# Kernel optimization log

Hardware: AMD Instinct MI355X
Metric: run time of the kernel (lower is better)

The kernel has to match this reference:

```python
import jax, jax.numpy as jnp
import numpy as np

EPS = 1e-4

def setup_inputs() -> dict:
    key = jax.random.key(0)
    k1, k2, k3 = jax.random.split(key, 3)
    batch, keysize, dict_size, categories = 4096, 512, 16384, 100
    x = jax.random.normal(k1, (batch, keysize), dtype=jnp.float32)
    keys = jax.random.normal(k2, (dict_size, keysize), dtype=jnp.float32) * 0.1  # TruncatedNormal(0, 0.1) approx
    values = jax.random.uniform(k3, (dict_size, categories), dtype=jnp.float32)
    return {"x": x, "keys": keys, "values": values}


def reference(x, keys, values):
    # sq_distance(keys, x): (dict_size, batch)
    kk = jnp.sum(keys * keys, axis=1)[:, None]          # (D, 1)
    xx = jnp.sum(x * x, axis=1)[None, :]                # (1, B)
    d = kk - 2.0 * jnp.matmul(keys, x.T) + xx           # (D, B)
    kern = 1.0 / (d + EPS)                              # reciprocal kernel
    # transpose -> (B, D), matmul values (D, C) -> (B, C)
    return jnp.matmul(kern.T, values)
```

## Files before the change

kernel.cpp:

```cpp
#include <hip/hip_runtime.h>
#include <hip/hip_bf16.h>
#include <hip/hip_fp8.h>
#include <cstdint>


#define BSZ   4096
#define DSZ   16384
#define KSZ   512
#define CC    100
#define CP    128
#define EPSV  1e-4f

#define BM     64
#define BD     64
#define DSPLIT 8
#define DCHUNK (DSZ / DSPLIT)
#define NITER  (DCHUNK / BD)
#define KTS    72

typedef short  short8 __attribute__((ext_vector_type(8)));
typedef float  f32x4  __attribute__((ext_vector_type(4)));
typedef long   lng2   __attribute__((ext_vector_type(2)));
typedef unsigned int   u32;
typedef unsigned short u16;
typedef unsigned char  u8;

__device__ __forceinline__ u16 f2bf(float f) {
    union { float f; u32 u; } cv; cv.f = f;
    u32 u = cv.u;
    u += 0x7fffu + ((u >> 16) & 1u);
    return (u16)(u >> 16);
}
__device__ __forceinline__ u32 pack2(float a, float b) {
    return (u32)f2bf(a) | ((u32)f2bf(b) << 16);
}
__device__ __forceinline__ u8 f2fp8(float f) {
    __hip_fp8_e4m3 t(f);
    return *reinterpret_cast<u8*>(&t);
}

__device__ __forceinline__ void gload_lds16(const void* g, void* l) {
    __builtin_amdgcn_global_load_lds(
        (const __attribute__((address_space(1))) u32*)g,
        (__attribute__((address_space(3))) u32*)l, 16, 0, 0);
}


__global__ __launch_bounds__(256)
void convert_xk(const float* __restrict__ x, const float* __restrict__ keys,
                u8* __restrict__ xw, u8* __restrict__ kw,
                float* __restrict__ kk, float* __restrict__ xx)
{
    const int tid = threadIdx.x, wid = tid >> 6, lane = tid & 63;
    const int row = blockIdx.x * 4 + wid;
    const float* src; u8* dst; float* nrm; int r;
    if (row < DSZ) { r = row;       src = keys + (size_t)r * KSZ; dst = kw + (size_t)r * KSZ; nrm = kk + r; }
    else           { r = row - DSZ; src = x    + (size_t)r * KSZ; dst = xw + (size_t)r * KSZ; nrm = xx + r; }

    float4 v0 = *reinterpret_cast<const float4*>(src + lane * 8);
    float4 v1 = *reinterpret_cast<const float4*>(src + lane * 8 + 4);
    float s = v0.x*v0.x + v0.y*v0.y + v0.z*v0.z + v0.w*v0.w
            + v1.x*v1.x + v1.y*v1.y + v1.z*v1.z + v1.w*v1.w;

    unsigned long long pk = 0;
    pk |= (unsigned long long)f2fp8(v0.x);
    pk |= (unsigned long long)f2fp8(v0.y) << 8;
    pk |= (unsigned long long)f2fp8(v0.z) << 16;
    pk |= (unsigned long long)f2fp8(v0.w) << 24;
    pk |= (unsigned long long)f2fp8(v1.x) << 32;
    pk |= (unsigned long long)f2fp8(v1.y) << 40;
    pk |= (unsigned long long)f2fp8(v1.z) << 48;
    pk |= (unsigned long long)f2fp8(v1.w) << 56;

    const int j = lane >> 2, hi_l = lane & 3;
    const int ch = j >> 3, jl = j & 7, jj = jl >> 1, f = jl & 1;
    const int off = ch * 256 + (((jj * 64 + hi_l * 16)) ^ ((r & 7) << 4)) + f * 8;
    *reinterpret_cast<unsigned long long*>(dst + off) = pk;

    s += __shfl_xor(s, 1);  s += __shfl_xor(s, 2);  s += __shfl_xor(s, 4);
    s += __shfl_xor(s, 8);  s += __shfl_xor(s, 16); s += __shfl_xor(s, 32);
    if (lane == 0) *nrm = s;
}

__global__ __launch_bounds__(256)
void convert_v(const float* __restrict__ values, u16* __restrict__ vw)
{
    const int gid = blockIdx.x * 256 + threadIdx.x;
    const int c = gid >> 11;
    const int j = gid & 2047;
    const int dp  = ((j >> 3) << 6) + ((j & 7) << 3);
    const int dsg = ((j >> 3) << 6) + (((j & 7) ^ (c & 7)) << 3);
    uint4 w = make_uint4(0, 0, 0, 0);
    if (c < CC) {
        float f[8];
#pragma unroll
        for (int i = 0; i < 8; ++i) f[i] = values[(size_t)(dsg + i) * CC + c];
        w.x = pack2(f[0], f[1]); w.y = pack2(f[2], f[3]);
        w.z = pack2(f[4], f[5]); w.w = pack2(f[6], f[7]);
    }
    *reinterpret_cast<uint4*>(vw + (size_t)c * DSZ + dp) = w;
}

__global__ __launch_bounds__(512, 4)
void varkeys_fast(const u8* __restrict__ xw, const u8* __restrict__ kw,
                  const u16* __restrict__ vw, const float* __restrict__ kkp,
                  const float* __restrict__ xxp, float* __restrict__ out)
{
    __shared__ __align__(16) u8  ksb0[BD * 256];
    __shared__ __align__(16) u8  ksb1[BD * 256];
    __shared__ __align__(16) u8  ksb2[BD * 256];
    __shared__ __align__(16) u16 kT[BM * KTS];
    __shared__ __align__(16) u16 vT[CP * BD];
    __shared__ float xx_s[BM];

    const int tid  = threadIdx.x;
    const int wid  = tid >> 6;
    const int lane = tid & 63;
    const int lo   = lane & 15;
    const int hi   = lane >> 4;
    const int wm   = wid >> 1;
    const int wn   = wid & 1;

    const int h  = blockIdx.x;
    const int by = h & 7, bx = h >> 3;
    const int bm0   = bx * BM;
    const int dbase = by * DCHUNK;

    if (tid < BM) xx_s[tid] = xxp[bm0 + tid];

    lng2 xq[8];
    {
        const int row = bm0 + wm * 16 + lo;
        const u8* base = xw + (size_t)row * KSZ;
        const int s16 = (row & 7) << 4;
#pragma unroll
        for (int ch = 0; ch < 2; ++ch)
#pragma unroll
            for (int jj = 0; jj < 4; ++jj)
                xq[ch * 4 + jj] = *reinterpret_cast<const lng2*>(
                    base + ch * 256 + ((jj * 64 + hi * 16) ^ s16));
    }

    f32x4 accO[4];
#pragma unroll
    for (int n = 0; n < 4; ++n) accO[n] = f32x4{0.f, 0.f, 0.f, 0.f};

#define IS_KS(BUFP, DK, CCH) { \
        _Pragma("unroll") \
        for (int i = 0; i < 2; ++i) { \
            const int ci = wid * 2 + i; \
            const int flat = ci * 1024 + lane * 16; \
            gload_lds16(kw + (size_t)((DK) + (flat >> 8)) * KSZ + (CCH) * 256 + (flat & 255), \
                        (char*)(BUFP) + ci * 1024); \
        } }

#define IS_VT(D0) { \
        _Pragma("unroll") \
        for (int i = 0; i < 2; ++i) { \
            const int ci = wid * 2 + i; \
            const int flat = ci * 512 + lane * 8; \
            gload_lds16(vw + (size_t)(flat >> 6) * DSZ + (D0) + (flat & 63), \
                        (char*)vT + ci * 1024); \
        } }

    IS_KS(ksb0, dbase, 0)
    IS_KS(ksb1, dbase, 1)
    asm volatile("s_waitcnt lgkmcnt(0)" ::: "memory");
    __builtin_amdgcn_s_barrier();

    const int swz   = (lo & 7) << 3;
    const int swz16 = (lo & 7) << 4;

#define A16(CH, BUF)                                                                  \
    {                                                                                 \
        _Pragma("unroll")                                                             \
        for (int jj = 0; jj < 4; ++jj) {                                              \
            const int off = (jj * 64 + hi * 16) ^ swz16;                              \
            const u8* p0 = (const u8*)(BUF) + (wn * 32 + lo) * 256 + off;             \
            lng2 b0 = *reinterpret_cast<const lng2*>(p0);                             \
            lng2 b1 = *reinterpret_cast<const lng2*>(p0 + 16 * 256);                  \
            lng2 a0 = xq[(CH) * 4 + jj];                                              \
            accS[0] = __builtin_amdgcn_mfma_f32_16x16x32_fp8_fp8(a0[0], b0[0], accS[0], 0, 0, 0); \
            accS[1] = __builtin_amdgcn_mfma_f32_16x16x32_fp8_fp8(a0[0], b1[0], accS[1], 0, 0, 0); \
            accS[0] = __builtin_amdgcn_mfma_f32_16x16x32_fp8_fp8(a0[1], b0[1], accS[0], 0, 0, 0); \
            accS[1] = __builtin_amdgcn_mfma_f32_16x16x32_fp8_fp8(a0[1], b1[1], accS[1], 0, 0, 0); \
        }                                                                             \
    }

    u8 *bA = ksb0, *bB = ksb1, *bC = ksb2;

    for (int it = 0; it < NITER; ++it) {
        const int d0 = dbase + it * BD;
        const bool pf = (it < NITER - 1);

        f32x4 accS[2];
#pragma unroll
        for (int n = 0; n < 2; ++n) accS[n] = f32x4{0.f, 0.f, 0.f, 0.f};

        const float kkf0 = kkp[d0 + wn * 32 + lo];
        const float kkf1 = kkp[d0 + wn * 32 + 16 + lo];
        IS_VT(d0)
        if (pf) {
            IS_KS(bC, d0 + BD, 0)
            asm volatile("s_waitcnt vmcnt(6)" ::: "memory");
        } else {
            asm volatile("s_waitcnt vmcnt(4)" ::: "memory");
        }
        __builtin_amdgcn_s_barrier();
        __builtin_amdgcn_sched_barrier(0);

        A16(0, bA)

        if (pf) {
            __builtin_amdgcn_s_barrier();
            __builtin_amdgcn_sched_barrier(0);
            IS_KS(bA, d0 + BD, 1)
        }

        A16(1, bB)

        if (pf) { asm volatile("s_waitcnt vmcnt(6)" ::: "memory"); }
        else    { asm volatile("s_waitcnt vmcnt(2)" ::: "memory"); }
#pragma unroll
        for (int n = 0; n < 2; ++n) {
            const int dl = wn * 32 + n * 16 + lo;
            const float kkv = n ? kkf1 : kkf0;
#pragma unroll
            for (int r = 0; r < 4; ++r) {
                const int rowl = wm * 16 + hi * 4 + r;
                const float dsq = kkv + xx_s[rowl] - 2.f * accS[n][r] + EPSV;
                kT[rowl * KTS + dl] = f2bf(__builtin_amdgcn_rcpf(dsq));
            }
        }
        if (pf) { asm volatile("s_waitcnt vmcnt(4)" ::: "memory"); }
        else    { asm volatile("s_waitcnt vmcnt(0)" ::: "memory"); }
        asm volatile("s_waitcnt lgkmcnt(0)" ::: "memory");
        __builtin_amdgcn_s_barrier();
        __builtin_amdgcn_sched_barrier(0);

#pragma unroll
        for (int kst = 0; kst < 2; ++kst) {
            const int k0l = kst * 32 + hi * 8;
            const int k0v = k0l ^ swz;
            short8 a0 = *reinterpret_cast<const short8*>(&kT[(wm * 16 + lo) * KTS + k0l]);
#pragma unroll
            for (int nh = 0; nh < 2; ++nh) {
                short8 b0 = *reinterpret_cast<const short8*>(&vT[(wn * 64 + nh * 32 + lo) * BD + k0v]);
                short8 b1 = *reinterpret_cast<const short8*>(&vT[(wn * 64 + nh * 32 + 16 + lo) * BD + k0v]);
                accO[nh * 2 + 0] = __builtin_amdgcn_mfma_f32_16x16x32_bf16(a0, b0, accO[nh * 2 + 0], 0, 0, 0);
                accO[nh * 2 + 1] = __builtin_amdgcn_mfma_f32_16x16x32_bf16(a0, b1, accO[nh * 2 + 1], 0, 0, 0);
            }
        }

        u8* t = bC; bC = bB; bB = bA; bA = t;
    }

#pragma unroll
    for (int n = 0; n < 4; ++n) {
        const int c = wn * 64 + n * 16 + lo;
        if (c < CC) {
#pragma unroll
            for (int r = 0; r < 4; ++r) {
                const int b_ = bm0 + wm * 16 + hi * 4 + r;
                atomicAdd(&out[(size_t)b_ * CC + c], accO[n][r]);
            }
        }
    }
#undef IS_KS
#undef IS_VT
#undef A16
}


#define FBM 128
#define XS_STRIDE 72
#define KS_STRIDE 72
#define KT_STRIDE 72
#define VL_STRIDE 106
#define FKC 64
#define FNKC (KSZ / FKC)
#define FDSPLIT 8
#define FDCHUNK (DSZ / FDSPLIT)
#define FNITER  (FDCHUNK / BD)

__global__ __launch_bounds__(256)
void varkeys_pre(const float* __restrict__ x, const float* __restrict__ keys,
                 float* __restrict__ kk, float* __restrict__ xx)
{
    const int tid  = threadIdx.x;
    const int wid  = tid >> 6;
    const int lane = tid & 63;
    const int lo   = lane & 15;
    const int sub  = lane >> 4;
    const int row  = blockIdx.x * 16 + wid * 4 + sub;
    const float* src = (row < DSZ) ? keys + (size_t)row * KSZ
                                   : x + (size_t)(row - DSZ) * KSZ;
    float s = 0.f;
#pragma unroll
    for (int j = 0; j < 8; ++j) {
        float4 v = *reinterpret_cast<const float4*>(src + j * 64 + lo * 4);
        s += v.x * v.x + v.y * v.y + v.z * v.z + v.w * v.w;
    }
    s += __shfl_xor(s, 1); s += __shfl_xor(s, 2);
    s += __shfl_xor(s, 4); s += __shfl_xor(s, 8);
    if (lo == 0) {
        if (row < DSZ) kk[row] = s;
        else           xx[row - DSZ] = s;
    }
}

__global__ __launch_bounds__(256, 2)
void varkeys_main(const float* __restrict__ x, const float* __restrict__ keys,
                  const float* __restrict__ values, float* __restrict__ out,
                  const float* __restrict__ kk_ws, const float* __restrict__ xx_ws,
                  int use_ws)
{
    __shared__ __align__(16) u16 xs[FBM * XS_STRIDE];
    __shared__ __align__(16) u16 ks[BD * KS_STRIDE];
    __shared__ __align__(16) u16 kTf[FBM * KT_STRIDE];
    __shared__ __align__(16) u16 vls[BD * VL_STRIDE];
    __shared__ float kk_s[FDCHUNK];
    __shared__ float xx_s[FBM];

    const int tid  = threadIdx.x;
    const int wid  = tid >> 6;
    const int lane = tid & 63;
    const int lo   = lane & 15;
    const int hi   = lane >> 4;
    const int wm   = wid >> 1;
    const int wn   = wid & 1;
    const int bm0   = blockIdx.x * FBM;
    const int dbase = blockIdx.y * FDCHUNK;

    if (use_ws) {
        for (int i = tid; i < FDCHUNK; i += 256) kk_s[i] = kk_ws[dbase + i];
        if (tid < FBM) xx_s[tid] = xx_ws[bm0 + tid];
    } else {
        for (int rbase = wid * 4; rbase < FDCHUNK + FBM; rbase += 16) {
            const int row = rbase + hi;
            const float* src = (row < FDCHUNK)
                ? keys + (size_t)(dbase + row) * KSZ
                : x + (size_t)(bm0 + row - FDCHUNK) * KSZ;
            float s = 0.f;
#pragma unroll
            for (int j = 0; j < 8; ++j) {
                float4 v = *reinterpret_cast<const float4*>(src + j * 64 + lo * 4);
                s += v.x * v.x + v.y * v.y + v.z * v.z + v.w * v.w;
            }
            s += __shfl_xor(s, 1); s += __shfl_xor(s, 2);
            s += __shfl_xor(s, 4); s += __shfl_xor(s, 8);
            if (lo == 0) {
                if (row < FDCHUNK) kk_s[row] = s;
                else               xx_s[row - FDCHUNK] = s;
            }
        }
    }
    __syncthreads();

    f32x4 accO[4][4];
#pragma unroll
    for (int m = 0; m < 4; ++m)
#pragma unroll
        for (int n = 0; n < 4; ++n) accO[m][n] = f32x4{0.f, 0.f, 0.f, 0.f};

    for (int it = 0; it < FNITER; ++it) {
        const int d0 = dbase + it * BD;

        f32x4 accS[4][2];
#pragma unroll
        for (int m = 0; m < 4; ++m)
#pragma unroll
            for (int n = 0; n < 2; ++n) accS[m][n] = f32x4{0.f, 0.f, 0.f, 0.f};

        for (int kc = 0; kc < FNKC; ++kc) {
            __syncthreads();
#pragma unroll
            for (int j = 0; j < 8; ++j) {
                const int idx = tid + j * 256;
                const int row = idx >> 4, c4 = idx & 15;
                float4 v = *reinterpret_cast<const float4*>(
                    x + (size_t)(bm0 + row) * KSZ + kc * FKC + c4 * 4);
                u32* dst = reinterpret_cast<u32*>(&xs[row * XS_STRIDE + c4 * 4]);
                dst[0] = pack2(v.x, v.y); dst[1] = pack2(v.z, v.w);
            }
#pragma unroll
            for (int j = 0; j < 4; ++j) {
                const int idx = tid + j * 256;
                const int row = idx >> 4, c4 = idx & 15;
                float4 v = *reinterpret_cast<const float4*>(
                    keys + (size_t)(d0 + row) * KSZ + kc * FKC + c4 * 4);
                u32* dst = reinterpret_cast<u32*>(&ks[row * KS_STRIDE + c4 * 4]);
                dst[0] = pack2(v.x, v.y); dst[1] = pack2(v.z, v.w);
            }
            __syncthreads();
#pragma unroll
            for (int kst = 0; kst < 2; ++kst) {
                const int k0 = kst * 32 + hi * 8;
                short8 a[4], b[2];
#pragma unroll
                for (int m = 0; m < 4; ++m)
                    a[m] = *reinterpret_cast<const short8*>(
                        &xs[(wm * 64 + m * 16 + lo) * XS_STRIDE + k0]);
#pragma unroll
                for (int n = 0; n < 2; ++n)
                    b[n] = *reinterpret_cast<const short8*>(
                        &ks[(wn * 32 + n * 16 + lo) * KS_STRIDE + k0]);
#pragma unroll
                for (int m = 0; m < 4; ++m)
#pragma unroll
                    for (int n = 0; n < 2; ++n)
                        accS[m][n] = __builtin_amdgcn_mfma_f32_16x16x32_bf16(
                            a[m], b[n], accS[m][n], 0, 0, 0);
            }
        }

#pragma unroll
        for (int m = 0; m < 4; ++m)
#pragma unroll
            for (int n = 0; n < 2; ++n) {
                const int dl = wn * 32 + n * 16 + lo;
                const float kkv = kk_s[it * BD + dl];
#pragma unroll
                for (int r = 0; r < 4; ++r) {
                    const int bl = wm * 64 + m * 16 + hi * 4 + r;
                    const float dsq = kkv + xx_s[bl] - 2.f * accS[m][n][r] + EPSV;
                    kTf[bl * KT_STRIDE + dl] = f2bf(__builtin_amdgcn_rcpf(dsq));
                }
            }

#pragma unroll
        for (int j = 0; j < 7; ++j) {
            const int idx = tid + j * 256;
            if (idx < 1600) {
                const int row = idx / 25, c4 = idx % 25;
                float4 v = *reinterpret_cast<const float4*>(
                    values + (size_t)(d0 + row) * CC + c4 * 4);
                u32* dst = reinterpret_cast<u32*>(&vls[row * VL_STRIDE + c4 * 4]);
                dst[0] = pack2(v.x, v.y); dst[1] = pack2(v.z, v.w);
            }
        }
        __syncthreads();

#pragma unroll
        for (int ks2 = 0; ks2 < 2; ++ks2) {
            const int k0 = ks2 * 32 + hi * 8;
            short8 a[4], b[4];
#pragma unroll
            for (int m = 0; m < 4; ++m)
                a[m] = *reinterpret_cast<const short8*>(
                    &kTf[(wm * 64 + m * 16 + lo) * KT_STRIDE + k0]);
#pragma unroll
            for (int n = 0; n < 4; ++n) {
                const int c = wn * 64 + n * 16 + lo;
                short8 t = {0, 0, 0, 0, 0, 0, 0, 0};
                if (c < CC) {
#pragma unroll
                    for (int i = 0; i < 8; ++i)
                        t[i] = (short)vls[(k0 + i) * VL_STRIDE + c];
                }
                b[n] = t;
            }
#pragma unroll
            for (int m = 0; m < 4; ++m)
#pragma unroll
                for (int n = 0; n < 4; ++n)
                    accO[m][n] = __builtin_amdgcn_mfma_f32_16x16x32_bf16(
                        a[m], b[n], accO[m][n], 0, 0, 0);
        }
    }

#pragma unroll
    for (int m = 0; m < 4; ++m)
#pragma unroll
        for (int n = 0; n < 4; ++n) {
            const int c = wn * 64 + n * 16 + lo;
            if (c < CC) {
#pragma unroll
                for (int r = 0; r < 4; ++r) {
                    const int b_ = bm0 + wm * 64 + m * 16 + hi * 4 + r;
                    atomicAdd(&out[(size_t)b_ * CC + c], accO[m][n][r]);
                }
            }
        }
}

extern "C" void kernel_launch(void* const* d_in, const int* in_sizes, int n_in,
                              void* d_out, int out_size, void* d_ws, size_t ws_size,
                              hipStream_t stream) {
    const float* x      = (const float*)d_in[0];
    const float* keys   = (const float*)d_in[1];
    const float* values = (const float*)d_in[2];
    float* out = (float*)d_out;

    hipMemsetAsync(d_out, 0, (size_t)out_size * sizeof(float), stream);

    const size_t off_xw = 0;
    const size_t off_kw = off_xw + (size_t)BSZ * KSZ;
    const size_t off_vw = off_kw + (size_t)DSZ * KSZ;
    const size_t off_kk = off_vw + (size_t)CP * DSZ * 2;
    const size_t off_xx = off_kk + (size_t)DSZ * 4;
    const size_t need   = off_xx + (size_t)BSZ * 4;

    if (ws_size >= need) {
        u8*  xw = (u8*)((char*)d_ws + off_xw);
        u8*  kw = (u8*)((char*)d_ws + off_kw);
        u16* vw = (u16*)((char*)d_ws + off_vw);
        float* kk = (float*)((char*)d_ws + off_kk);
        float* xx = (float*)((char*)d_ws + off_xx);
        convert_xk<<<dim3((DSZ + BSZ) / 4), dim3(256), 0, stream>>>(x, keys, xw, kw, kk, xx);
        convert_v<<<dim3((CP * DSZ / 8) / 256), dim3(256), 0, stream>>>(values, vw);
        varkeys_fast<<<dim3(DSPLIT * (BSZ / BM)), dim3(512), 0, stream>>>(xw, kw, vw, kk, xx, out);
    } else {
        const size_t ws_need = (size_t)(DSZ + BSZ) * sizeof(float);
        const int use_ws = (ws_size >= ws_need) ? 1 : 0;
        float* kk = (float*)d_ws;
        float* xx = kk + DSZ;
        if (use_ws) {
            varkeys_pre<<<dim3((DSZ + BSZ) / 16), dim3(256), 0, stream>>>(x, keys, kk, xx);
        }
        varkeys_main<<<dim3(BSZ / FBM, FDSPLIT), dim3(256), 0, stream>>>(
            x, keys, values, out, kk, xx, use_ws);
    }
}
```

Measured before the change: 113.7 us.

## Remap waves to 2x4 grid so each wave covers two row tiles and shares B fragments

Changes the wave layout from 4x2 to 2x4. Each wave now handles two 16-row M tiles of x against one 16-column key tile, and two rows by two column tiles in the second GEMM. This halves the keys LDS reads per MFMA and lets A and B fragments be reused, at the cost of holding twice as many x fragments in registers. It also moves the xx norms, with eps folded in, into per-thread registers instead of shared memory. The V and K prefetch issue now comes after the barrier, so the vmcnt waits are restructured. That makes the pipelining and wait counts harder to check for correctness.

After: 121.7 us. 7.1% more time.

```diff
diff --git a/kernel.cpp b/kernel.cpp
--- a/kernel.cpp
+++ b/kernel.cpp
@@ -111,39 +111,45 @@
     __shared__ __align__(16) u8  ksb2[BD * 256];
     __shared__ __align__(16) u16 kT[BM * KTS];
     __shared__ __align__(16) u16 vT[CP * BD];
-    __shared__ float xx_s[BM];
 
     const int tid  = threadIdx.x;
     const int wid  = tid >> 6;
     const int lane = tid & 63;
     const int lo   = lane & 15;
     const int hi   = lane >> 4;
-    const int wm   = wid >> 1;
-    const int wn   = wid & 1;
+    const int wp   = wid >> 2;
+    const int wq   = wid & 3;
 
     const int h  = blockIdx.x;
     const int by = h & 7, bx = h >> 3;
     const int bm0   = bx * BM;
     const int dbase = by * DCHUNK;
 
-    if (tid < BM) xx_s[tid] = xxp[bm0 + tid];
-
-    lng2 xq[8];
-    {
-        const int row = bm0 + wm * 16 + lo;
+    lng2 xq[2][8];
+#pragma unroll
+    for (int m = 0; m < 2; ++m) {
+        const int row = bm0 + wp * 32 + m * 16 + lo;
         const u8* base = xw + (size_t)row * KSZ;
         const int s16 = (row & 7) << 4;
 #pragma unroll
         for (int ch = 0; ch < 2; ++ch)
 #pragma unroll
             for (int jj = 0; jj < 4; ++jj)
-                xq[ch * 4 + jj] = *reinterpret_cast<const lng2*>(
+                xq[m][ch * 4 + jj] = *reinterpret_cast<const lng2*>(
                     base + ch * 256 + ((jj * 64 + hi * 16) ^ s16));
     }
-
-    f32x4 accO[4];
-#pragma unroll
-    for (int n = 0; n < 4; ++n) accO[n] = f32x4{0.f, 0.f, 0.f, 0.f};
+    float xr[8];
+#pragma unroll
+    for (int m = 0; m < 2; ++m)
+#pragma unroll
+        for (int r = 0; r < 4; ++r)
+            xr[m * 4 + r] = xxp[bm0 + wp * 32 + m * 16 + hi * 4 + r] + EPSV;
+
+    f32x4 accO[2][2];
+#pragma unroll
+    for (int m = 0; m < 2; ++m)
+#pragma unroll
+        for (int n = 0; n < 2; ++n) accO[m][n] = f32x4{0.f, 0.f, 0.f, 0.f};
 
 #define IS_KS(BUFP, DK, CCH) { \
         _Pragma("unroll") \
@@ -165,7 +171,6 @@
 
     IS_KS(ksb0, dbase, 0)
     IS_KS(ksb1, dbase, 1)
-    asm volatile("s_waitcnt lgkmcnt(0)" ::: "memory");
     __builtin_amdgcn_s_barrier();
 
     const int swz   = (lo & 7) << 3;
@@ -176,14 +181,12 @@
         _Pragma("unroll")                                                             \
         for (int jj = 0; jj < 4; ++jj) {                                              \
             const int off = (jj * 64 + hi * 16) ^ swz16;                              \
-            const u8* p0 = (const u8*)(BUF) + (wn * 32 + lo) * 256 + off;             \
-            lng2 b0 = *reinterpret_cast<const lng2*>(p0);                             \
-            lng2 b1 = *reinterpret_cast<const lng2*>(p0 + 16 * 256);                  \
-            lng2 a0 = xq[(CH) * 4 + jj];                                              \
-            accS[0] = __builtin_amdgcn_mfma_f32_16x16x32_fp8_fp8(a0[0], b0[0], accS[0], 0, 0, 0); \
-            accS[1] = __builtin_amdgcn_mfma_f32_16x16x32_fp8_fp8(a0[0], b1[0], accS[1], 0, 0, 0); \
-            accS[0] = __builtin_amdgcn_mfma_f32_16x16x32_fp8_fp8(a0[1], b0[1], accS[0], 0, 0, 0); \
-            accS[1] = __builtin_amdgcn_mfma_f32_16x16x32_fp8_fp8(a0[1], b1[1], accS[1], 0, 0, 0); \
+            const u8* p0 = (const u8*)(BUF) + (wq * 16 + lo) * 256 + off;             \
+            lng2 b = *reinterpret_cast<const lng2*>(p0);                              \
+            accS[0] = __builtin_amdgcn_mfma_f32_16x16x32_fp8_fp8(xq[0][(CH) * 4 + jj][0], b[0], accS[0], 0, 0, 0); \
+            accS[1] = __builtin_amdgcn_mfma_f32_16x16x32_fp8_fp8(xq[1][(CH) * 4 + jj][0], b[0], accS[1], 0, 0, 0); \
+            accS[0] = __builtin_amdgcn_mfma_f32_16x16x32_fp8_fp8(xq[0][(CH) * 4 + jj][1], b[1], accS[0], 0, 0, 0); \
+            accS[1] = __builtin_amdgcn_mfma_f32_16x16x32_fp8_fp8(xq[1][(CH) * 4 + jj][1], b[1], accS[1], 0, 0, 0); \
         }                                                                             \
     }
 
@@ -197,17 +200,12 @@
 #pragma unroll
         for (int n = 0; n < 2; ++n) accS[n] = f32x4{0.f, 0.f, 0.f, 0.f};
 
-        const float kkf0 = kkp[d0 + wn * 32 + lo];
-        const float kkf1 = kkp[d0 + wn * 32 + 16 + lo];
-        IS_VT(d0)
-        if (pf) {
-            IS_KS(bC, d0 + BD, 0)
-            asm volatile("s_waitcnt vmcnt(6)" ::: "memory");
-        } else {
-            asm volatile("s_waitcnt vmcnt(4)" ::: "memory");
-        }
+        const float kkf = kkp[d0 + wq * 16 + lo];
+        asm volatile("s_waitcnt vmcnt(1)" ::: "memory");
         __builtin_amdgcn_s_barrier();
         __builtin_amdgcn_sched_barrier(0);
+        IS_VT(d0)
+        if (pf) IS_KS(bC, d0 + BD, 0)
 
         A16(0, bA)
 
@@ -221,16 +219,16 @@
 
         if (pf) { asm volatile("s_waitcnt vmcnt(6)" ::: "memory"); }
         else    { asm volatile("s_waitcnt vmcnt(2)" ::: "memory"); }
-#pragma unroll
-        for (int n = 0; n < 2; ++n) {
-            const int dl = wn * 32 + n * 16 + lo;
-            const float kkv = n ? kkf1 : kkf0;
-#pragma unroll
-            for (int r = 0; r < 4; ++r) {
-                const int rowl = wm * 16 + hi * 4 + r;
-                const float dsq = kkv + xx_s[rowl] - 2.f * accS[n][r] + EPSV;
-                kT[rowl * KTS + dl] = f2bf(__builtin_amdgcn_rcpf(dsq));
-            }
+        {
+            const int dl = wq * 16 + lo;
+#pragma unroll
+            for (int m = 0; m < 2; ++m)
+#pragma unroll
+                for (int r = 0; r < 4; ++r) {
+                    const int rowl = wp * 32 + m * 16 + hi * 4 + r;
+                    const float dsq = kkf + xr[m * 4 + r] - 2.f * accS[m][r];
+                    kT[rowl * KTS + dl] = f2bf(__builtin_amdgcn_rcpf(dsq));
+                }
         }
         if (pf) { asm volatile("s_waitcnt vmcnt(4)" ::: "memory"); }
         else    { asm volatile("s_waitcnt vmcnt(0)" ::: "memory"); }
@@ -242,30 +240,32 @@
         for (int kst = 0; kst < 2; ++kst) {
             const int k0l = kst * 32 + hi * 8;
             const int k0v = k0l ^ swz;
-            short8 a0 = *reinterpret_cast<const short8*>(&kT[(wm * 16 + lo) * KTS + k0l]);
-#pragma unroll
-            for (int nh = 0; nh < 2; ++nh) {
-                short8 b0 = *reinterpret_cast<const short8*>(&vT[(wn * 64 + nh * 32 + lo) * BD + k0v]);
-                short8 b1 = *reinterpret_cast<const short8*>(&vT[(wn * 64 + nh * 32 + 16 + lo) * BD + k0v]);
-                accO[nh * 2 + 0] = __builtin_amdgcn_mfma_f32_16x16x32_bf16(a0, b0, accO[nh * 2 + 0], 0, 0, 0);
-                accO[nh * 2 + 1] = __builtin_amdgcn_mfma_f32_16x16x32_bf16(a0, b1, accO[nh * 2 + 1], 0, 0, 0);
-            }
+            short8 a0 = *reinterpret_cast<const short8*>(&kT[(wp * 32 + lo) * KTS + k0l]);
+            short8 a1 = *reinterpret_cast<const short8*>(&kT[(wp * 32 + 16 + lo) * KTS + k0l]);
+            short8 b0 = *reinterpret_cast<const short8*>(&vT[(wq * 32 + lo) * BD + k0v]);
+            short8 b1 = *reinterpret_cast<const short8*>(&vT[(wq * 32 + 16 + lo) * BD + k0v]);
+            accO[0][0] = __builtin_amdgcn_mfma_f32_16x16x32_bf16(a0, b0, accO[0][0], 0, 0, 0);
+            accO[1][0] = __builtin_amdgcn_mfma_f32_16x16x32_bf16(a1, b0, accO[1][0], 0, 0, 0);
+            accO[0][1] = __builtin_amdgcn_mfma_f32_16x16x32_bf16(a0, b1, accO[0][1], 0, 0, 0);
+            accO[1][1] = __builtin_amdgcn_mfma_f32_16x16x32_bf16(a1, b1, accO[1][1], 0, 0, 0);
         }
 
         u8* t = bC; bC = bB; bB = bA; bA = t;
     }
 
 #pragma unroll
-    for (int n = 0; n < 4; ++n) {
-        const int c = wn * 64 + n * 16 + lo;
-        if (c < CC) {
-#pragma unroll
-            for (int r = 0; r < 4; ++r) {
-                const int b_ = bm0 + wm * 16 + hi * 4 + r;
-                atomicAdd(&out[(size_t)b_ * CC + c], accO[n][r]);
-            }
-        }
-    }
+    for (int m = 0; m < 2; ++m)
+#pragma unroll
+        for (int nn = 0; nn < 2; ++nn) {
+            const int c = wq * 32 + nn * 16 + lo;
+            if (c < CC) {
+#pragma unroll
+                for (int r = 0; r < 4; ++r) {
+                    const int b_ = bm0 + wp * 32 + m * 16 + hi * 4 + r;
+                    atomicAdd(&out[(size_t)b_ * CC + c], accO[m][nn][r]);
+                }
+            }
+        }
 #undef IS_KS
 #undef IS_VT
 #undef A16
```
